# Kernel optimization log

Hardware: AMD Instinct MI355X
Metric: run time of the kernel (lower is better)

The kernel has to match this reference:

```python
import jax, jax.numpy as jnp
import numpy as np

NEG_SLOPE = 0.2  # PyG GATConv default leaky_relu slope


def gat_conv(x, src, dst, n, W, a_src, a_dst, b):
    """Single-head PyG GATConv (self-loops already included in src/dst)."""
    h = x @ W                                  # [N, F]
    alpha_s = h @ a_src                        # [N]
    alpha_d = h @ a_dst                        # [N]
    e = jax.nn.leaky_relu(alpha_s[src] + alpha_d[dst], NEG_SLOPE)  # [E]
    m = jax.ops.segment_max(e, dst, num_segments=n)
    e = jnp.exp(e - m[dst])
    s = jax.ops.segment_sum(e, dst, num_segments=n)
    alpha = e / s[dst]                         # softmax over incoming edges
    out = jax.ops.segment_sum(alpha[:, None] * h[src], dst, num_segments=n)
    return out + b


def setup_inputs() -> dict:
    key = jax.random.key(0)
    ks = jax.random.split(key, 12)
    N, E = 8192, 262144
    IN, H, OUT, K = 512, 128, 64, 16
    x = jax.random.normal(ks[0], (N, IN), dtype=jnp.float32)
    edge_index = jax.random.randint(ks[1], (2, E), 0, N, dtype=jnp.int32)
    def glorot(k, shape):
        lim = np.sqrt(6.0 / (shape[0] + shape[-1]))
        return jax.random.uniform(k, shape, jnp.float32, -lim, lim)
    return {
        "x": x,
        "edge_index": edge_index,
        "W1": glorot(ks[2], (IN, H)),
        "a_src1": glorot(ks[3], (H,)),
        "a_dst1": glorot(ks[4], (H,)),
        "b1": jnp.zeros((H,), jnp.float32),
        "W2": glorot(ks[5], (H, OUT)),
        "a_src2": glorot(ks[6], (OUT,)),
        "a_dst2": glorot(ks[7], (OUT,)),
        "b2": jnp.zeros((OUT,), jnp.float32),
        "centers": glorot(ks[8], (K, OUT)),
    }


def reference(x, edge_index, W1, a_src1, a_dst1, b1, W2, a_src2, a_dst2, b2, centers):
    n = x.shape[0]
    # add self loops (PyG GATConv default add_self_loops=True)
    loop = jnp.arange(n, dtype=edge_index.dtype)
    src = jnp.concatenate([edge_index[0], loop])
    dst = jnp.concatenate([edge_index[1], loop])
    h = jax.nn.elu(gat_conv(x, src, dst, n, W1, a_src1, a_dst1, b1))
    z = gat_conv(h, src, dst, n, W2, a_src2, a_dst2, b2)       # [N, D]
    A_pred = jax.nn.sigmoid(z @ z.T)                            # [N, N]
    # Student-t soft assignment: [N, K]
    d2 = jnp.sum((z[:, None, :] - centers[None, :, :]) ** 2, axis=2)
    q = 1.0 / (1.0 + d2)
    q = q / jnp.sum(q, axis=1, keepdims=True)
    return (z, A_pred, q)
```

## Files before the change

kernel.cpp:

```cpp
#include <hip/hip_runtime.h>
#include <hip/hip_bf16.h>

typedef __bf16 v8bf __attribute__((ext_vector_type(8)));
typedef float  v4f  __attribute__((ext_vector_type(4)));

__device__ __forceinline__ float lrelu02(float x){ return x > 0.f ? x : 0.2f*x; }

__device__ __forceinline__ unsigned short f2bf_rn(float f){
  unsigned int u = __float_as_uint(f);
  u += 0x7fffu + ((u >> 16) & 1u);
  return (unsigned short)(u >> 16);
}
__device__ __forceinline__ float bf2f(unsigned short h){
  return __uint_as_float(((unsigned int)h) << 16);
}

__global__ void zero_int_kernel(int* p, int n){
  int i = blockIdx.x*blockDim.x + threadIdx.x;
  if (i < n) p[i] = 0;
}

__global__ void hist_kernel(const int* __restrict__ dst, int* counts, int E){
  int i = blockIdx.x*blockDim.x + threadIdx.x;
  if (i < E) atomicAdd(&counts[dst[i]], 1);
}

__global__ void scan_kernel(const int* __restrict__ counts, int* ptr, int* cursor, int n){
  __shared__ int sd[1024];
  int t = threadIdx.x;
  int base = t*8;
  int v[8]; int s = 0;
  #pragma unroll
  for (int i = 0; i < 8; ++i){ int x = (base+i < n) ? counts[base+i] : 0; v[i] = x; s += x; }
  sd[t] = s; __syncthreads();
  for (int off = 1; off < 1024; off <<= 1){
    int x = (t >= off) ? sd[t-off] : 0;
    __syncthreads();
    sd[t] += x;
    __syncthreads();
  }
  int run = sd[t] - s;
  #pragma unroll
  for (int i = 0; i < 8; ++i){
    if (base+i < n){ ptr[base+i] = run; cursor[base+i] = run; run += v[i]; }
  }
  if (t == 1023) ptr[n] = run;
}

__global__ void scatter_kernel(const int* __restrict__ src, const int* __restrict__ dst,
                               int* cursor, int* csr_src, int E){
  int i = blockIdx.x*blockDim.x + threadIdx.x;
  if (i < E){
    int p = atomicAdd(&cursor[dst[i]], 1);
    csr_src[p] = src[i];
  }
}

__global__ void convert_kernel(const float* __restrict__ x, const float* __restrict__ W1,
    unsigned short* xh, unsigned short* xl, unsigned short* wth, unsigned short* wtl,
    int nx, int nw){
  int i = blockIdx.x*blockDim.x + threadIdx.x;
  if (i < nx){
    float f = x[i];
    unsigned short h = f2bf_rn(f);
    xh[i] = h;
    xl[i] = f2bf_rn(f - bf2f(h));
  } else if (i < nx + nw){
    int e = i - nx;
    int k = e >> 7, n = e & 127;
    float f = W1[e];
    unsigned short h = f2bf_rn(f);
    wth[n*512 + k] = h;
    wtl[n*512 + k] = f2bf_rn(f - bf2f(h));
  }
}

__global__ __launch_bounds__(128) void gemm1_mfma(const unsigned short* __restrict__ xh,
    const unsigned short* __restrict__ xl, const unsigned short* __restrict__ wth,
    const unsigned short* __restrict__ wtl, float* __restrict__ h1){
  const int lane = threadIdx.x & 63;
  const int wave = threadIdx.x >> 6;
  const int i0 = blockIdx.x*32 + wave*16;
  const int r = lane & 15, q = lane >> 4;
  const unsigned short* xrh = xh + (size_t)(i0 + r)*512;
  const unsigned short* xrl = xl + (size_t)(i0 + r)*512;
  v4f acc[8];
  #pragma unroll
  for (int c = 0; c < 8; ++c) acc[c] = (v4f){0.f,0.f,0.f,0.f};
  for (int kt = 0; kt < 16; ++kt){
    int k = kt*32 + q*8;
    v8bf ah = *reinterpret_cast<const v8bf*>(xrh + k);
    v8bf al = *reinterpret_cast<const v8bf*>(xrl + k);
    #pragma unroll
    for (int ct = 0; ct < 8; ++ct){
      v8bf bh = *reinterpret_cast<const v8bf*>(wth + (size_t)(ct*16 + r)*512 + k);
      v8bf bl = *reinterpret_cast<const v8bf*>(wtl + (size_t)(ct*16 + r)*512 + k);
      acc[ct] = __builtin_amdgcn_mfma_f32_16x16x32_bf16(ah, bh, acc[ct], 0,0,0);
      acc[ct] = __builtin_amdgcn_mfma_f32_16x16x32_bf16(al, bh, acc[ct], 0,0,0);
      acc[ct] = __builtin_amdgcn_mfma_f32_16x16x32_bf16(ah, bl, acc[ct], 0,0,0);
    }
  }
  #pragma unroll
  for (int ct = 0; ct < 8; ++ct)
    #pragma unroll
    for (int t = 0; t < 4; ++t)
      h1[(size_t)(i0 + q*4 + t)*128 + ct*16 + r] = acc[ct][t];
}

template<int BM,int BN,int BK,int TM,int TN>
__global__ __launch_bounds__(256) void gemm_tiled(const float* __restrict__ A,
    const float* __restrict__ B, float* __restrict__ C, int M, int N, int K){
  __shared__ float As[BK][BM+1];
  __shared__ float Bs[BK][BN+1];
  const int tid = threadIdx.x;
  const int tx = tid % (BN/TN);
  const int ty = tid / (BN/TN);
  const int brow = blockIdx.y*BM;
  const int bcol = blockIdx.x*BN;
  float acc[TM][TN] = {};
  for (int k0 = 0; k0 < K; k0 += BK){
    for (int i = tid; i < BM*BK; i += 256){
      int m = i / BK, kk = i % BK;
      As[kk][m] = A[(size_t)(brow+m)*K + k0 + kk];
    }
    for (int i = tid; i < BK*BN; i += 256){
      int kk = i / BN, nn = i % BN;
      Bs[kk][nn] = B[(size_t)(k0+kk)*N + bcol + nn];
    }
    __syncthreads();
    #pragma unroll
    for (int kk = 0; kk < BK; ++kk){
      float a[TM], b[TN];
      #pragma unroll
      for (int m = 0; m < TM; ++m) a[m] = As[kk][ty*TM+m];
      #pragma unroll
      for (int n = 0; n < TN; ++n) b[n] = Bs[kk][tx*TN+n];
      #pragma unroll
      for (int m = 0; m < TM; ++m)
        #pragma unroll
        for (int n = 0; n < TN; ++n) acc[m][n] += a[m]*b[n];
    }
    __syncthreads();
  }
  #pragma unroll
  for (int m = 0; m < TM; ++m)
    #pragma unroll
    for (int n = 0; n < TN; ++n)
      C[(size_t)(brow+ty*TM+m)*N + bcol+tx*TN+n] = acc[m][n];
}

__global__ void alpha_kernel(const float* __restrict__ h, const float* __restrict__ avs,
                             const float* __restrict__ avd, float* as_out, float* ad_out,
                             int n, int F){
  int wid = (blockIdx.x*blockDim.x + threadIdx.x) >> 6;
  int lane = threadIdx.x & 63;
  if (wid >= n) return;
  float ps = 0.f, pd = 0.f;
  for (int c = lane; c < F; c += 64){
    float hv = h[(size_t)wid*F + c];
    ps += hv * avs[c];
    pd += hv * avd[c];
  }
  for (int o = 32; o; o >>= 1){ ps += __shfl_xor(ps, o); pd += __shfl_xor(pd, o); }
  if (lane == 0){ as_out[wid] = ps; ad_out[wid] = pd; }
}

__global__ void gat_agg1(const float* __restrict__ h, const float* __restrict__ as,
                         const float* __restrict__ ad, const int* __restrict__ ptr,
                         const int* __restrict__ csr_src, const float* __restrict__ bias,
                         float* __restrict__ out, int n){
  const int F = 128;
  int wid = (blockIdx.x*blockDim.x + threadIdx.x) >> 6;
  int lane = threadIdx.x & 63;
  if (wid >= n) return;
  const int v = wid;
  const int beg = ptr[v], end = ptr[v+1];
  const float adv = ad[v];
  const float asv = as[v];
  float m = lrelu02(asv + adv);
  for (int j = beg + lane; j < end; j += 64)
    m = fmaxf(m, lrelu02(as[csr_src[j]] + adv));
  for (int o = 32; o; o >>= 1) m = fmaxf(m, __shfl_xor(m, o));
  float acc0 = 0.f, acc1 = 0.f, ssum = 0.f;
  float wself = __expf(lrelu02(asv + adv) - m);
  if (lane == 0) ssum += wself;
  acc0 += wself * h[(size_t)v*F + lane];
  acc1 += wself * h[(size_t)v*F + 64 + lane];
  for (int b0 = beg; b0 < end; b0 += 64){
    int j = b0 + lane;
    float wv = 0.f; int sv = 0;
    if (j < end){
      sv = csr_src[j];
      wv = __expf(lrelu02(as[sv] + adv) - m);
      ssum += wv;
    }
    int cnt = min(64, end - b0);
    for (int t = 0; t < cnt; ++t){
      float wt = __shfl(wv, t);
      int   st = __shfl(sv, t);
      acc0 += wt * h[(size_t)st*F + lane];
      acc1 += wt * h[(size_t)st*F + 64 + lane];
    }
  }
  for (int o = 32; o; o >>= 1) ssum += __shfl_xor(ssum, o);
  float inv = 1.f / ssum;
  float r0 = acc0*inv + bias[lane];
  r0 = r0 > 0.f ? r0 : __expf(r0) - 1.f;
  out[(size_t)v*F + lane] = r0;
  float r1 = acc1*inv + bias[64 + lane];
  r1 = r1 > 0.f ? r1 : __expf(r1) - 1.f;
  out[(size_t)v*F + 64 + lane] = r1;
}

__global__ void gat_agg2_fused(const float* __restrict__ h, const float* __restrict__ as,
                               const float* __restrict__ ad, const int* __restrict__ ptr,
                               const int* __restrict__ csr_src, const float* __restrict__ bias,
                               const float* __restrict__ centers,
                               float* __restrict__ z_out, unsigned short* __restrict__ zhi,
                               unsigned short* __restrict__ zlo, float* __restrict__ qout,
                               int n, int K){
  const int F = 64;
  int wid = (blockIdx.x*blockDim.x + threadIdx.x) >> 6;
  int lane = threadIdx.x & 63;
  if (wid >= n) return;
  const int v = wid;
  const int beg = ptr[v], end = ptr[v+1];
  const float adv = ad[v];
  const float asv = as[v];
  float m = lrelu02(asv + adv);
  for (int j = beg + lane; j < end; j += 64)
    m = fmaxf(m, lrelu02(as[csr_src[j]] + adv));
  for (int o = 32; o; o >>= 1) m = fmaxf(m, __shfl_xor(m, o));
  float acc0 = 0.f, ssum = 0.f;
  float wself = __expf(lrelu02(asv + adv) - m);
  if (lane == 0) ssum += wself;
  acc0 += wself * h[(size_t)v*F + lane];
  for (int b0 = beg; b0 < end; b0 += 64){
    int j = b0 + lane;
    float wv = 0.f; int sv = 0;
    if (j < end){
      sv = csr_src[j];
      wv = __expf(lrelu02(as[sv] + adv) - m);
      ssum += wv;
    }
    int cnt = min(64, end - b0);
    for (int t = 0; t < cnt; ++t){
      float wt = __shfl(wv, t);
      int   st = __shfl(sv, t);
      acc0 += wt * h[(size_t)st*F + lane];
    }
  }
  for (int o = 32; o; o >>= 1) ssum += __shfl_xor(ssum, o);
  float r0 = acc0 / ssum + bias[lane];
  z_out[(size_t)v*F + lane] = r0;
  unsigned short hh = f2bf_rn(r0);
  zhi[(size_t)v*F + lane] = hh;
  zlo[(size_t)v*F + lane] = f2bf_rn(r0 - bf2f(hh));
  float myq = 0.f, tot = 0.f;
  for (int k = 0; k < K; ++k){
    float d = r0 - centers[k*F + lane];
    float d2 = d*d;
    for (int o = 32; o; o >>= 1) d2 += __shfl_xor(d2, o);
    float qq = 1.f / (1.f + d2);
    if (lane == k) myq = qq;
    tot += qq;
  }
  if (lane < K) qout[(size_t)v*K + lane] = myq / tot;
}

__device__ __forceinline__ v8bf ldz(const unsigned short* z, int node, int k){
  return *reinterpret_cast<const v8bf*>(z + ((size_t)node << 6) + k);
}

__global__ __launch_bounds__(256) void apred_kernel(const unsigned short* __restrict__ zhi,
    const unsigned short* __restrict__ zlo, float* __restrict__ out, int N){
  __shared__ float tile[4][16][68];
  const int lane = threadIdx.x & 63;
  const int wave = threadIdx.x >> 6;
  const int i0 = blockIdx.y*64 + wave*16;
  const int j0 = blockIdx.x*64;
  const int r = lane & 15, q = lane >> 4;
  const int arow = i0 + r;
  v8bf ahi0 = ldz(zhi, arow,      q*8);
  v8bf ahi1 = ldz(zhi, arow, 32 + q*8);
  v8bf alo0 = ldz(zlo, arow,      q*8);
  v8bf alo1 = ldz(zlo, arow, 32 + q*8);
  #pragma unroll
  for (int c = 0; c < 4; ++c){
    int brow = j0 + c*16 + r;
    v8bf bhi0 = ldz(zhi, brow,      q*8);
    v8bf bhi1 = ldz(zhi, brow, 32 + q*8);
    v8bf blo0 = ldz(zlo, brow,      q*8);
    v8bf blo1 = ldz(zlo, brow, 32 + q*8);
    v4f acc = {0.f,0.f,0.f,0.f};
    acc = __builtin_amdgcn_mfma_f32_16x16x32_bf16(ahi0, bhi0, acc, 0,0,0);
    acc = __builtin_amdgcn_mfma_f32_16x16x32_bf16(ahi1, bhi1, acc, 0,0,0);
    acc = __builtin_amdgcn_mfma_f32_16x16x32_bf16(ahi0, blo0, acc, 0,0,0);
    acc = __builtin_amdgcn_mfma_f32_16x16x32_bf16(ahi1, blo1, acc, 0,0,0);
    acc = __builtin_amdgcn_mfma_f32_16x16x32_bf16(alo0, bhi0, acc, 0,0,0);
    acc = __builtin_amdgcn_mfma_f32_16x16x32_bf16(alo1, bhi1, acc, 0,0,0);
    #pragma unroll
    for (int t = 0; t < 4; ++t){
      float e = __expf(-acc[t]);
      tile[wave][q*4 + t][c*16 + r] = __builtin_amdgcn_rcpf(1.f + e);
    }
  }
  #pragma unroll
  for (int t = 0; t < 4; ++t){
    int row = t*4 + (lane >> 4);
    int col = (lane & 15)*4;
    v4f vv = *reinterpret_cast<v4f*>(&tile[wave][row][col]);
    *reinterpret_cast<v4f*>(out + (size_t)(i0 + row)*N + j0 + col) = vv;
  }
}

extern "C" void kernel_launch(void* const* d_in, const int* in_sizes, int n_in,
                              void* d_out, int out_size, void* d_ws, size_t ws_size,
                              hipStream_t stream) {
  const float* x      = (const float*)d_in[0];
  const int*   ei     = (const int*)  d_in[1];
  const float* W1     = (const float*)d_in[2];
  const float* a_src1 = (const float*)d_in[3];
  const float* a_dst1 = (const float*)d_in[4];
  const float* b1     = (const float*)d_in[5];
  const float* W2     = (const float*)d_in[6];
  const float* a_src2 = (const float*)d_in[7];
  const float* a_dst2 = (const float*)d_in[8];
  const float* b2     = (const float*)d_in[9];
  const float* cent   = (const float*)d_in[10];

  const int H   = in_sizes[3];
  const int OUTF= in_sizes[7];
  const int INF = in_sizes[2] / H;
  const int N   = in_sizes[0] / INF;
  const int E   = in_sizes[1] / 2;
  const int K   = in_sizes[10] / OUTF;

  const int* e_src = ei;
  const int* e_dst = ei + E;

  char* wsp = (char*)d_ws;
  auto alloc = [&](size_t b)->void*{ void* p = (void*)wsp; wsp += (b + 255) & ~(size_t)255; return p; };
  int* counts   = (int*)alloc((size_t)N*4);
  int* ptr      = (int*)alloc((size_t)(N+1)*4);
  int* cursor   = (int*)alloc((size_t)N*4);
  int* csr_src  = (int*)alloc((size_t)E*4);
  float* as1    = (float*)alloc((size_t)N*4);
  float* ad1    = (float*)alloc((size_t)N*4);
  float* as2    = (float*)alloc((size_t)N*4);
  float* ad2    = (float*)alloc((size_t)N*4);
  unsigned short* zhi = (unsigned short*)alloc((size_t)N*OUTF*2);
  unsigned short* zlo = (unsigned short*)alloc((size_t)N*OUTF*2);
  unsigned short* xh  = (unsigned short*)alloc((size_t)N*INF*2);
  unsigned short* xl  = (unsigned short*)alloc((size_t)N*INF*2);
  unsigned short* wth = (unsigned short*)alloc((size_t)INF*H*2);
  unsigned short* wtl = (unsigned short*)alloc((size_t)INF*H*2);

  float* out_f  = (float*)d_out;
  float* z_out  = out_f;
  float* ap_out = out_f + (size_t)N*OUTF;
  float* q_out  = ap_out + (size_t)N*N;
  float* h1  = ap_out;
  float* h2  = h1 + (size_t)N*H;
  float* h2w = h2 + (size_t)N*H;

  const int wavesPerGrid = (N*64 + 255)/256;
  const int nx = N*INF, nw = INF*H;

  zero_int_kernel<<<(N+255)/256, 256, 0, stream>>>(counts, N);
  hist_kernel<<<(E+255)/256, 256, 0, stream>>>(e_dst, counts, E);
  scan_kernel<<<1, 1024, 0, stream>>>(counts, ptr, cursor, N);
  scatter_kernel<<<(E+255)/256, 256, 0, stream>>>(e_src, e_dst, cursor, csr_src, E);
  convert_kernel<<<(nx+nw+255)/256, 256, 0, stream>>>(x, W1, xh, xl, wth, wtl, nx, nw);
  gemm1_mfma<<<N/32, 128, 0, stream>>>(xh, xl, wth, wtl, h1);
  alpha_kernel<<<wavesPerGrid, 256, 0, stream>>>(h1, a_src1, a_dst1, as1, ad1, N, H);
  gat_agg1<<<wavesPerGrid, 256, 0, stream>>>(h1, as1, ad1, ptr, csr_src, b1, h2, N);
  gemm_tiled<64,64,16,4,4><<<dim3(OUTF/64, N/64), 256, 0, stream>>>(h2, W2, h2w, N, OUTF, H);
  alpha_kernel<<<wavesPerGrid, 256, 0, stream>>>(h2w, a_src2, a_dst2, as2, ad2, N, OUTF);
  gat_agg2_fused<<<wavesPerGrid, 256, 0, stream>>>(h2w, as2, ad2, ptr, csr_src, b2, cent,
                                                   z_out, zhi, zlo, q_out, N, K);
  apred_kernel<<<dim3(N/64, N/64), 256, 0, stream>>>(zhi, zlo, ap_out, N);
}
```

Before: 562.5 us.

## Fuse input conversion and attention dots into GEMMs, vectorize aggregation gathers

Removes the separate x bf16 split pass by converting fp32 x inside the MFMA GEMM, and folds the per-node attention dot products into both GEMM epilogues, eliminating two alpha kernels. The count zeroing is merged with the W1 conversion. The aggregation loops are changed to process several neighbors per wave with float4 gathers, followed by cross-lane reductions. A_pred stores become nontemporal. Together these cut launches and intermediate traffic, at the cost of redundant x conversion across waves and extra shuffle work.

```diff
diff --git a/kernel.cpp b/kernel.cpp
--- a/kernel.cpp
+++ b/kernel.cpp
@@ -2,6 +2,7 @@
 #include <hip/hip_bf16.h>
 
 typedef __bf16 v8bf __attribute__((ext_vector_type(8)));
+typedef unsigned short v8us __attribute__((ext_vector_type(8)));
 typedef float  v4f  __attribute__((ext_vector_type(4)));
 
 __device__ __forceinline__ float lrelu02(float x){ return x > 0.f ? x : 0.2f*x; }
@@ -15,10 +16,7 @@
   return __uint_as_float(((unsigned int)h) << 16);
 }
 
-__global__ void zero_int_kernel(int* p, int n){
-  int i = blockIdx.x*blockDim.x + threadIdx.x;
-  if (i < n) p[i] = 0;
-}
+union BF8cast { v8us u; v8bf b; };
 
 __global__ void hist_kernel(const int* __restrict__ dst, int* counts, int E){
   int i = blockIdx.x*blockDim.x + threadIdx.x;
@@ -56,41 +54,47 @@
   }
 }
 
-__global__ void convert_kernel(const float* __restrict__ x, const float* __restrict__ W1,
-    unsigned short* xh, unsigned short* xl, unsigned short* wth, unsigned short* wtl,
-    int nx, int nw){
+__global__ void prep_kernel(const float* __restrict__ W1,
+    unsigned short* wth, unsigned short* wtl, int* counts, int nw, int n){
   int i = blockIdx.x*blockDim.x + threadIdx.x;
-  if (i < nx){
-    float f = x[i];
+  if (i < nw){
+    int k = i >> 7, c = i & 127;
+    float f = W1[i];
     unsigned short h = f2bf_rn(f);
-    xh[i] = h;
-    xl[i] = f2bf_rn(f - bf2f(h));
-  } else if (i < nx + nw){
-    int e = i - nx;
-    int k = e >> 7, n = e & 127;
-    float f = W1[e];
-    unsigned short h = f2bf_rn(f);
-    wth[n*512 + k] = h;
-    wtl[n*512 + k] = f2bf_rn(f - bf2f(h));
-  }
-}
-
-__global__ __launch_bounds__(128) void gemm1_mfma(const unsigned short* __restrict__ xh,
-    const unsigned short* __restrict__ xl, const unsigned short* __restrict__ wth,
-    const unsigned short* __restrict__ wtl, float* __restrict__ h1){
+    wth[c*512 + k] = h;
+    wtl[c*512 + k] = f2bf_rn(f - bf2f(h));
+  } else if (i < nw + n){
+    counts[i - nw] = 0;
+  }
+}
+
+__global__ __launch_bounds__(128) void gemm1_fused(const float* __restrict__ x,
+    const unsigned short* __restrict__ wth, const unsigned short* __restrict__ wtl,
+    const float* __restrict__ avs, const float* __restrict__ avd,
+    float* __restrict__ h1, float* __restrict__ as_out, float* __restrict__ ad_out){
   const int lane = threadIdx.x & 63;
   const int wave = threadIdx.x >> 6;
   const int i0 = blockIdx.x*32 + wave*16;
   const int r = lane & 15, q = lane >> 4;
-  const unsigned short* xrh = xh + (size_t)(i0 + r)*512;
-  const unsigned short* xrl = xl + (size_t)(i0 + r)*512;
+  const float* xr = x + (size_t)(i0 + r)*512;
   v4f acc[8];
   #pragma unroll
   for (int c = 0; c < 8; ++c) acc[c] = (v4f){0.f,0.f,0.f,0.f};
   for (int kt = 0; kt < 16; ++kt){
     int k = kt*32 + q*8;
-    v8bf ah = *reinterpret_cast<const v8bf*>(xrh + k);
-    v8bf al = *reinterpret_cast<const v8bf*>(xrl + k);
+    v4f xa = *reinterpret_cast<const v4f*>(xr + k);
+    v4f xb = *reinterpret_cast<const v4f*>(xr + k + 4);
+    v8us ahu, alu;
+    #pragma unroll
+    for (int j = 0; j < 8; ++j){
+      float f = (j < 4) ? xa[j] : xb[j-4];
+      unsigned short hh = f2bf_rn(f);
+      ahu[j] = hh;
+      alu[j] = f2bf_rn(f - bf2f(hh));
+    }
+    BF8cast ch; ch.u = ahu;
+    BF8cast cl; cl.u = alu;
+    v8bf ah = ch.b, al = cl.b;
     #pragma unroll
     for (int ct = 0; ct < 8; ++ct){
       v8bf bh = *reinterpret_cast<const v8bf*>(wth + (size_t)(ct*16 + r)*512 + k);
@@ -105,64 +109,28 @@
     #pragma unroll
     for (int t = 0; t < 4; ++t)
       h1[(size_t)(i0 + q*4 + t)*128 + ct*16 + r] = acc[ct][t];
-}
-
-template<int BM,int BN,int BK,int TM,int TN>
-__global__ __launch_bounds__(256) void gemm_tiled(const float* __restrict__ A,
-    const float* __restrict__ B, float* __restrict__ C, int M, int N, int K){
-  __shared__ float As[BK][BM+1];
-  __shared__ float Bs[BK][BN+1];
-  const int tid = threadIdx.x;
-  const int tx = tid % (BN/TN);
-  const int ty = tid / (BN/TN);
-  const int brow = blockIdx.y*BM;
-  const int bcol = blockIdx.x*BN;
-  float acc[TM][TN] = {};
-  for (int k0 = 0; k0 < K; k0 += BK){
-    for (int i = tid; i < BM*BK; i += 256){
-      int m = i / BK, kk = i % BK;
-      As[kk][m] = A[(size_t)(brow+m)*K + k0 + kk];
-    }
-    for (int i = tid; i < BK*BN; i += 256){
-      int kk = i / BN, nn = i % BN;
-      Bs[kk][nn] = B[(size_t)(k0+kk)*N + bcol + nn];
-    }
-    __syncthreads();
-    #pragma unroll
-    for (int kk = 0; kk < BK; ++kk){
-      float a[TM], b[TN];
-      #pragma unroll
-      for (int m = 0; m < TM; ++m) a[m] = As[kk][ty*TM+m];
-      #pragma unroll
-      for (int n = 0; n < TN; ++n) b[n] = Bs[kk][tx*TN+n];
-      #pragma unroll
-      for (int m = 0; m < TM; ++m)
-        #pragma unroll
-        for (int n = 0; n < TN; ++n) acc[m][n] += a[m]*b[n];
-    }
-    __syncthreads();
-  }
-  #pragma unroll
-  for (int m = 0; m < TM; ++m)
-    #pragma unroll
-    for (int n = 0; n < TN; ++n)
-      C[(size_t)(brow+ty*TM+m)*N + bcol+tx*TN+n] = acc[m][n];
-}
-
-__global__ void alpha_kernel(const float* __restrict__ h, const float* __restrict__ avs,
-                             const float* __restrict__ avd, float* as_out, float* ad_out,
-                             int n, int F){
-  int wid = (blockIdx.x*blockDim.x + threadIdx.x) >> 6;
-  int lane = threadIdx.x & 63;
-  if (wid >= n) return;
-  float ps = 0.f, pd = 0.f;
-  for (int c = lane; c < F; c += 64){
-    float hv = h[(size_t)wid*F + c];
-    ps += hv * avs[c];
-    pd += hv * avd[c];
-  }
-  for (int o = 32; o; o >>= 1){ ps += __shfl_xor(ps, o); pd += __shfl_xor(pd, o); }
-  if (lane == 0){ as_out[wid] = ps; ad_out[wid] = pd; }
+  float sa[4] = {0.f,0.f,0.f,0.f}, da[4] = {0.f,0.f,0.f,0.f};
+  #pragma unroll
+  for (int ct = 0; ct < 8; ++ct){
+    float ws = avs[ct*16 + r], wd = avd[ct*16 + r];
+    #pragma unroll
+    for (int t = 0; t < 4; ++t){ sa[t] += acc[ct][t]*ws; da[t] += acc[ct][t]*wd; }
+  }
+  #pragma unroll
+  for (int off = 1; off < 16; off <<= 1){
+    #pragma unroll
+    for (int t = 0; t < 4; ++t){
+      sa[t] += __shfl_xor(sa[t], off);
+      da[t] += __shfl_xor(da[t], off);
+    }
+  }
+  if (r == 0){
+    #pragma unroll
+    for (int t = 0; t < 4; ++t){
+      as_out[i0 + q*4 + t] = sa[t];
+      ad_out[i0 + q*4 + t] = da[t];
+    }
+  }
 }
 
 __global__ void gat_agg1(const float* __restrict__ h, const float* __restrict__ as,
@@ -181,11 +149,14 @@
   for (int j = beg + lane; j < end; j += 64)
     m = fmaxf(m, lrelu02(as[csr_src[j]] + adv));
   for (int o = 32; o; o >>= 1) m = fmaxf(m, __shfl_xor(m, o));
-  float acc0 = 0.f, acc1 = 0.f, ssum = 0.f;
+  const int half = lane >> 5, l32 = lane & 31;
+  v4f acc = (v4f){0.f,0.f,0.f,0.f};
   float wself = __expf(lrelu02(asv + adv) - m);
-  if (lane == 0) ssum += wself;
-  acc0 += wself * h[(size_t)v*F + lane];
-  acc1 += wself * h[(size_t)v*F + 64 + lane];
+  float ssum = (lane == 0) ? wself : 0.f;
+  if (half == 0){
+    v4f hv = *reinterpret_cast<const v4f*>(h + (size_t)v*F + l32*4);
+    acc += hv * wself;
+  }
   for (int b0 = beg; b0 < end; b0 += 64){
     int j = b0 + lane;
     float wv = 0.f; int sv = 0;
@@ -195,21 +166,94 @@
       ssum += wv;
     }
     int cnt = min(64, end - b0);
-    for (int t = 0; t < cnt; ++t){
-      float wt = __shfl(wv, t);
-      int   st = __shfl(sv, t);
-      acc0 += wt * h[(size_t)st*F + lane];
-      acc1 += wt * h[(size_t)st*F + 64 + lane];
+    for (int t = 0; t < cnt; t += 2){
+      int idx = t + half;
+      float wt = __shfl(wv, idx);
+      int   st = __shfl(sv, idx);
+      if (idx >= cnt){ wt = 0.f; st = v; }
+      v4f hv = *reinterpret_cast<const v4f*>(h + (size_t)st*F + l32*4);
+      acc += hv * wt;
     }
   }
   for (int o = 32; o; o >>= 1) ssum += __shfl_xor(ssum, o);
-  float inv = 1.f / ssum;
-  float r0 = acc0*inv + bias[lane];
-  r0 = r0 > 0.f ? r0 : __expf(r0) - 1.f;
-  out[(size_t)v*F + lane] = r0;
-  float r1 = acc1*inv + bias[64 + lane];
-  r1 = r1 > 0.f ? r1 : __expf(r1) - 1.f;
-  out[(size_t)v*F + 64 + lane] = r1;
+  #pragma unroll
+  for (int c = 0; c < 4; ++c) acc[c] += __shfl_xor(acc[c], 32);
+  if (half == 0){
+    float inv = 1.f / ssum;
+    v4f bv = *reinterpret_cast<const v4f*>(bias + l32*4);
+    v4f rr;
+    #pragma unroll
+    for (int c = 0; c < 4; ++c){
+      float r0 = acc[c]*inv + bv[c];
+      rr[c] = r0 > 0.f ? r0 : __expf(r0) - 1.f;
+    }
+    *reinterpret_cast<v4f*>(out + (size_t)v*F + l32*4) = rr;
+  }
+}
+
+template<int BM,int BN,int BK,int TM,int TN>
+__global__ __launch_bounds__(256) void gemm2_fused(const float* __restrict__ A,
+    const float* __restrict__ B, float* __restrict__ C, int M, int N, int K,
+    const float* __restrict__ avs, const float* __restrict__ avd,
+    float* __restrict__ as_out, float* __restrict__ ad_out){
+  __shared__ float As[BK][BM+1];
+  __shared__ float Bs[BK][BN+1];
+  __shared__ float reds[BM][17];
+  __shared__ float redd[BM][17];
+  const int tid = threadIdx.x;
+  const int tx = tid % (BN/TN);
+  const int ty = tid / (BN/TN);
+  const int brow = blockIdx.y*BM;
+  const int bcol = blockIdx.x*BN;
+  float acc[TM][TN] = {};
+  for (int k0 = 0; k0 < K; k0 += BK){
+    for (int i = tid; i < BM*BK; i += 256){
+      int m = i / BK, kk = i % BK;
+      As[kk][m] = A[(size_t)(brow+m)*K + k0 + kk];
+    }
+    for (int i = tid; i < BK*BN; i += 256){
+      int kk = i / BN, nn = i % BN;
+      Bs[kk][nn] = B[(size_t)(k0+kk)*N + bcol + nn];
+    }
+    __syncthreads();
+    #pragma unroll
+    for (int kk = 0; kk < BK; ++kk){
+      float a[TM], b[TN];
+      #pragma unroll
+      for (int m = 0; m < TM; ++m) a[m] = As[kk][ty*TM+m];
+      #pragma unroll
+      for (int n = 0; n < TN; ++n) b[n] = Bs[kk][tx*TN+n];
+      #pragma unroll
+      for (int m = 0; m < TM; ++m)
+        #pragma unroll
+        for (int n = 0; n < TN; ++n) acc[m][n] += a[m]*b[n];
+    }
+    __syncthreads();
+  }
+  float ps[TM] = {}, pd[TM] = {};
+  #pragma unroll
+  for (int m = 0; m < TM; ++m){
+    #pragma unroll
+    for (int n = 0; n < TN; ++n){
+      float c = acc[m][n];
+      C[(size_t)(brow+ty*TM+m)*N + bcol+tx*TN+n] = c;
+      float s = avs[bcol+tx*TN+n], d = avd[bcol+tx*TN+n];
+      ps[m] += c*s; pd[m] += c*d;
+    }
+  }
+  #pragma unroll
+  for (int m = 0; m < TM; ++m){
+    reds[ty*TM+m][tx] = ps[m];
+    redd[ty*TM+m][tx] = pd[m];
+  }
+  __syncthreads();
+  if (tid < BM){
+    float s = 0.f, d = 0.f;
+    #pragma unroll
+    for (int k = 0; k < BN/TN; ++k){ s += reds[tid][k]; d += redd[tid][k]; }
+    as_out[brow + tid] = s;
+    ad_out[brow + tid] = d;
+  }
 }
 
 __global__ void gat_agg2_fused(const float* __restrict__ h, const float* __restrict__ as,
@@ -231,10 +275,14 @@
   for (int j = beg + lane; j < end; j += 64)
     m = fmaxf(m, lrelu02(as[csr_src[j]] + adv));
   for (int o = 32; o; o >>= 1) m = fmaxf(m, __shfl_xor(m, o));
-  float acc0 = 0.f, ssum = 0.f;
+  const int qr = lane >> 4, l16 = lane & 15;
+  v4f acc = (v4f){0.f,0.f,0.f,0.f};
   float wself = __expf(lrelu02(asv + adv) - m);
-  if (lane == 0) ssum += wself;
-  acc0 += wself * h[(size_t)v*F + lane];
+  float ssum = (lane == 0) ? wself : 0.f;
+  if (qr == 0){
+    v4f hv = *reinterpret_cast<const v4f*>(h + (size_t)v*F + l16*4);
+    acc += hv * wself;
+  }
   for (int b0 = beg; b0 < end; b0 += 64){
     int j = b0 + lane;
     float wv = 0.f; int sv = 0;
@@ -244,14 +292,29 @@
       ssum += wv;
     }
     int cnt = min(64, end - b0);
-    for (int t = 0; t < cnt; ++t){
-      float wt = __shfl(wv, t);
-      int   st = __shfl(sv, t);
-      acc0 += wt * h[(size_t)st*F + lane];
+    for (int t = 0; t < cnt; t += 4){
+      int idx = t + qr;
+      float wt = __shfl(wv, idx);
+      int   st = __shfl(sv, idx);
+      if (idx >= cnt){ wt = 0.f; st = v; }
+      v4f hv = *reinterpret_cast<const v4f*>(h + (size_t)st*F + l16*4);
+      acc += hv * wt;
     }
   }
   for (int o = 32; o; o >>= 1) ssum += __shfl_xor(ssum, o);
-  float r0 = acc0 / ssum + bias[lane];
+  #pragma unroll
+  for (int c = 0; c < 4; ++c){
+    acc[c] += __shfl_xor(acc[c], 16);
+    acc[c] += __shfl_xor(acc[c], 32);
+  }
+  int srcLane = lane >> 2;
+  float c0 = __shfl(acc[0], srcLane);
+  float c1 = __shfl(acc[1], srcLane);
+  float c2 = __shfl(acc[2], srcLane);
+  float c3 = __shfl(acc[3], srcLane);
+  int sel = lane & 3;
+  float av = sel == 0 ? c0 : sel == 1 ? c1 : sel == 2 ? c2 : c3;
+  float r0 = av / ssum + bias[lane];
   z_out[(size_t)v*F + lane] = r0;
   unsigned short hh = f2bf_rn(r0);
   zhi[(size_t)v*F + lane] = hh;
@@ -310,7 +373,7 @@
     int row = t*4 + (lane >> 4);
     int col = (lane & 15)*4;
     v4f vv = *reinterpret_cast<v4f*>(&tile[wave][row][col]);
-    *reinterpret_cast<v4f*>(out + (size_t)(i0 + row)*N + j0 + col) = vv;
+    __builtin_nontemporal_store(vv, reinterpret_cast<v4f*>(out + (size_t)(i0 + row)*N + j0 + col));
   }
 }
 
@@ -351,8 +414,6 @@
   float* ad2    = (float*)alloc((size_t)N*4);
   unsigned short* zhi = (unsigned short*)alloc((size_t)N*OUTF*2);
   unsigned short* zlo = (unsigned short*)alloc((size_t)N*OUTF*2);
-  unsigned short* xh  = (unsigned short*)alloc((size_t)N*INF*2);
-  unsigned short* xl  = (unsigned short*)alloc((size_t)N*INF*2);
   unsigned short* wth = (unsigned short*)alloc((size_t)INF*H*2);
   unsigned short* wtl = (unsigned short*)alloc((size_t)INF*H*2);
 
@@ -365,18 +426,16 @@
   float* h2w = h2 + (size_t)N*H;
 
   const int wavesPerGrid = (N*64 + 255)/256;
-  const int nx = N*INF, nw = INF*H;
-
-  zero_int_kernel<<<(N+255)/256, 256, 0, stream>>>(counts, N);
+  const int nw = INF*H;
+
+  prep_kernel<<<(nw + N + 255)/256, 256, 0, stream>>>(W1, wth, wtl, counts, nw, N);
   hist_kernel<<<(E+255)/256, 256, 0, stream>>>(e_dst, counts, E);
   scan_kernel<<<1, 1024, 0, stream>>>(counts, ptr, cursor, N);
   scatter_kernel<<<(E+255)/256, 256, 0, stream>>>(e_src, e_dst, cursor, csr_src, E);
-  convert_kernel<<<(nx+nw+255)/256, 256, 0, stream>>>(x, W1, xh, xl, wth, wtl, nx, nw);
-  gemm1_mfma<<<N/32, 128, 0, stream>>>(xh, xl, wth, wtl, h1);
-  alpha_kernel<<<wavesPerGrid, 256, 0, stream>>>(h1, a_src1, a_dst1, as1, ad1, N, H);
+  gemm1_fused<<<N/32, 128, 0, stream>>>(x, wth, wtl, a_src1, a_dst1, h1, as1, ad1);
   gat_agg1<<<wavesPerGrid, 256, 0, stream>>>(h1, as1, ad1, ptr, csr_src, b1, h2, N);
-  gemm_tiled<64,64,16,4,4><<<dim3(OUTF/64, N/64), 256, 0, stream>>>(h2, W2, h2w, N, OUTF, H);
-  alpha_kernel<<<wavesPerGrid, 256, 0, stream>>>(h2w, a_src2, a_dst2, as2, ad2, N, OUTF);
+  gemm2_fused<64,64,16,4,4><<<dim3(OUTF/64, N/64), 256, 0, stream>>>(h2, W2, h2w, N, OUTF, H,
+                                                                     a_src2, a_dst2, as2, ad2);
   gat_agg2_fused<<<wavesPerGrid, 256, 0, stream>>>(h2w, as2, ad2, ptr, csr_src, b2, cent,
                                                    z_out, zhi, zlo, q_out, N, K);
   apred_kernel<<<dim3(N/64, N/64), 256, 0, stream>>>(zhi, zlo, ap_out, N);
```

Result: faster. 546.1 us (-2.9%).
